# Optimization experiments

Hardware: AMD Instinct MI355X
Metric: run time of the kernel (lower is better)

The kernel has to match this reference:

```python
import jax, jax.numpy as jnp
import numpy as np

V = 8001
H = 512
B = 64
T = 129  # seq len; model unrolls T-1 steps
EPS = 1e-5
P_DROP = 0.3


def setup_inputs() -> dict:
    key = jax.random.key(0)
    ks = jax.random.split(key, 16)
    s = 1.0 / np.sqrt(H)
    inp = {
        "x": jax.random.randint(ks[0], (B, T), 0, V),
        "emb": jax.random.normal(ks[1], (V, H), jnp.float32) * 0.1,
        "W_ih1": jax.random.normal(ks[2], (4 * H, H), jnp.float32) * s,
        "W_hh1": jax.random.normal(ks[3], (4 * H, H), jnp.float32) * s,
        "b_ih1": jax.random.normal(ks[4], (4 * H,), jnp.float32) * s,
        "b_hh1": jax.random.normal(ks[5], (4 * H,), jnp.float32) * s,
        "gamma1": jnp.ones((H,), jnp.float32),
        "beta1": jnp.zeros((H,), jnp.float32),
        "mask1": (jax.random.bernoulli(ks[6], 1 - P_DROP, (B, H)).astype(jnp.float32) / (1 - P_DROP)),
        "W_ih2": jax.random.normal(ks[7], (4 * H, H), jnp.float32) * s,
        "W_hh2": jax.random.normal(ks[8], (4 * H, H), jnp.float32) * s,
        "b_ih2": jax.random.normal(ks[9], (4 * H,), jnp.float32) * s,
        "b_hh2": jax.random.normal(ks[10], (4 * H,), jnp.float32) * s,
        "gamma2": jnp.ones((H,), jnp.float32),
        "beta2": jnp.zeros((H,), jnp.float32),
        "mask2": (jax.random.bernoulli(ks[11], 1 - P_DROP, (B, H)).astype(jnp.float32) / (1 - P_DROP)),
        "W_dec": jax.random.normal(ks[12], (V, H), jnp.float32) * s,
        "b_dec": jax.random.normal(ks[13], (V,), jnp.float32) * s,
    }
    return inp


def _lstm_cell(xt, h, c, W_ih, W_hh, b_ih, b_hh):
    # PyTorch LSTMCell gate packing: i, f, g, o
    gates = xt @ W_ih.T + b_ih + h @ W_hh.T + b_hh  # [B, 4H]
    i, f, g, o = jnp.split(gates, 4, axis=-1)
    c_new = jax.nn.sigmoid(f) * c + jax.nn.sigmoid(i) * jnp.tanh(g)
    h_new = jax.nn.sigmoid(o) * jnp.tanh(c_new)
    return h_new, c_new


def _batchnorm(h, gamma, beta):
    # training-mode BatchNorm1d: biased batch stats over batch dim
    mu = h.mean(axis=0)
    var = h.var(axis=0)
    return gamma * (h - mu) * jax.lax.rsqrt(var + EPS) + beta


def reference(x, emb, W_ih1, W_hh1, b_ih1, b_hh1, gamma1, beta1, mask1,
              W_ih2, W_hh2, b_ih2, b_hh2, gamma2, beta2, mask2, W_dec, b_dec):
    embed = emb[x]                              # [B, T, H]
    xs = jnp.swapaxes(embed[:, :-1, :], 0, 1)   # [T-1, B, H]

    def step(carry, xt):
        h1, c1, h2, c2 = carry
        h1, c1 = _lstm_cell(xt, h1, c1, W_ih1, W_hh1, b_ih1, b_hh1)
        a = _batchnorm(h1, gamma1, beta1) * mask1
        h2, c2 = _lstm_cell(a, h2, c2, W_ih2, W_hh2, b_ih2, b_hh2)
        b = _batchnorm(h2, gamma2, beta2) * mask2
        out = b @ W_dec.T + b_dec               # [B, V]
        return (h1, c1, h2, c2), out

    z = jnp.zeros((B, H), embed.dtype)
    _, outs = jax.lax.scan(step, (z, z, z, z), xs)  # [T-1, B, V]
    return jnp.transpose(outs, (1, 2, 0))           # [B, V, T-1]
```

## Files before the change

kernel.cpp:

```cpp
#include <hip/hip_runtime.h>

typedef __attribute__((ext_vector_type(8))) short bf16x8;
typedef __attribute__((ext_vector_type(4))) float f32x4;

#define NBATCH 64
#define NH     512
#define NV     8001
#define NVP    8064
#define NSTEP  128
#define NG     2048
#define SLAB   32768

#define OFF_XS    ((size_t)0)
#define SZ_XS     ((size_t)NSTEP*SLAB*2)
#define OFF_WP    (OFF_XS + SZ_XS)
#define SZ_WP     ((size_t)2*2048*1024*2)
#define OFF_WDEC  (OFF_WP + SZ_WP)
#define SZ_WDEC   ((size_t)NVP*NH*2)
#define OFF_BIAS  (OFF_WDEC + SZ_WDEC)
#define SZ_BIAS   ((size_t)2*NG*4)
#define OFF_H1    (OFF_BIAS + SZ_BIAS)
#define SZ_H1     ((size_t)(NSTEP+1)*SLAB*2)
#define OFF_AB    (OFF_H1 + SZ_H1)
#define SZ_AB     ((size_t)NSTEP*SLAB*2)
#define OFF_H2    (OFF_AB + SZ_AB)
#define SZ_H2     ((size_t)(NSTEP+1)*SLAB*2)
#define OFF_BSEQ  (OFF_H2 + SZ_H2)
#define SZ_BSEQ   ((size_t)NSTEP*SLAB*2)
#define OFF_BAR   (OFF_BSEQ + SZ_BSEQ)
#define SZ_BAR    ((size_t)65536)

#define F_D1(t)   ((t) * 32)
#define F_D2(t)   (4096 + (t) * 32)
#define F_QCNT    8192
#define F_GBAR    8224
#define F_DRDY(c) (8320 + (c) * 32)

__device__ __forceinline__ unsigned short f2bf(float x) {
  union { float f; unsigned u; } v; v.f = x;
  unsigned r = v.u + 0x7FFFu + ((v.u >> 16) & 1u);
  return (unsigned short)(r >> 16);
}
__device__ __forceinline__ float sigm(float x) { return 1.f / (1.f + __expf(-x)); }

template <int SLP>
__device__ __forceinline__ void waitflag(unsigned* f) {
  while (__hip_atomic_load(f, __ATOMIC_RELAXED, __HIP_MEMORY_SCOPE_AGENT) < 32u)
    __builtin_amdgcn_s_sleep(SLP);
  asm volatile("" ::: "memory");
}

template <int SLP>
__device__ __forceinline__ void waitone(unsigned* f) {
  if (!__hip_atomic_load(f, __ATOMIC_RELAXED, __HIP_MEMORY_SCOPE_AGENT)) {
    do { __builtin_amdgcn_s_sleep(SLP); }
    while (!__hip_atomic_load(f, __ATOMIC_RELAXED, __HIP_MEMORY_SCOPE_AGENT));
  }
  asm volatile("" ::: "memory");
}

struct KArgs {
  const int* x; const float* emb;
  const float* Wih1; const float* Whh1; const float* bi1; const float* bh1;
  const float* g1; const float* be1; const float* m1;
  const float* Wih2; const float* Whh2; const float* bi2; const float* bh2;
  const float* g2; const float* be2; const float* m2;
  const float* Wdec; const float* bdec;
  unsigned short* xs; unsigned short* wp; unsigned short* wdec; float* bias;
  unsigned short* h1q; unsigned short* abq; unsigned short* h2q; unsigned short* bseq;
  unsigned* bar; float* out;
};

__global__ void __launch_bounds__(256, 1) k_main(KArgs a) {
  __shared__ unsigned short wlds[32 * 4 * 64 * 8];
  __shared__ float red[4][2][16];

  unsigned* bar = a.bar;
  const int bid = blockIdx.x;
  const int lane = threadIdx.x & 63, w = threadIdx.x >> 6;
  const int q = lane >> 4, n = lane & 15;

  {
    const int gtid = bid * 256 + threadIdx.x;
    if (gtid < 4096)
      a.bias[gtid] = (gtid < NG) ? (a.bi1[gtid] + a.bh1[gtid])
                                 : (a.bi2[gtid - NG] + a.bh2[gtid - NG]);
    if (gtid < 4096) {
      ((uint4*)a.h1q)[gtid] = (uint4){0, 0, 0, 0};
      ((uint4*)a.h2q)[gtid] = (uint4){0, 0, 0, 0};
    }
    for (int i = gtid; i < 524288; i += 65536) {
      int t = i >> 12, b = (i >> 6) & 63, h8 = i & 63;
      const float* src = a.emb + (size_t)a.x[b * 129 + t] * NH + h8 * 8;
      float4 u = *(const float4*)src, v = *(const float4*)(src + 4);
      unsigned short tmp[8] = {f2bf(u.x), f2bf(u.y), f2bf(u.z), f2bf(u.w),
                               f2bf(v.x), f2bf(v.y), f2bf(v.z), f2bf(v.w)};
      *(uint4*)(a.xs + (size_t)i * 8) = *(const uint4*)tmp;
    }
    for (int i = gtid; i < 516096; i += 65536) {
      int v = i >> 6, h8 = i & 63;
      unsigned short tmp[8] = {0, 0, 0, 0, 0, 0, 0, 0};
      if (v < NV) {
        const float* src = a.Wdec + (size_t)v * NH + h8 * 8;
        float4 u = *(const float4*)src, vv = *(const float4*)(src + 4);
        tmp[0] = f2bf(u.x); tmp[1] = f2bf(u.y); tmp[2] = f2bf(u.z); tmp[3] = f2bf(u.w);
        tmp[4] = f2bf(vv.x); tmp[5] = f2bf(vv.y); tmp[6] = f2bf(vv.z); tmp[7] = f2bf(vv.w);
      }
      *(uint4*)(a.wdec + (size_t)i * 8) = *(const uint4*)tmp;
    }
    for (int i = gtid; i < 524288; i += 65536) {
      int l = i & 63, g = (i >> 6) & 3, s = (i >> 8) & 31, lb = (i >> 13) & 31, layer = i >> 18;
      int nn = l & 15, qq = l >> 4;
      int r = g * NH + lb * 16 + nn;
      int k0 = s * 32 + qq * 8;
      const float* Wih = layer ? a.Wih2 : a.Wih1;
      const float* Whh = layer ? a.Whh2 : a.Whh1;
      const float* src = (k0 < NH) ? (Wih + (size_t)r * NH + k0) : (Whh + (size_t)r * NH + (k0 - NH));
      unsigned short tmp[8];
#pragma unroll
      for (int j = 0; j < 8; ++j) tmp[j] = f2bf(src[j]);
      *(uint4*)(a.wp + (size_t)i * 8) = *(const uint4*)tmp;
    }
  }
  __syncthreads();
  if (threadIdx.x == 0) {
    __builtin_amdgcn_fence(__ATOMIC_RELEASE, "agent");
    __hip_atomic_fetch_add(bar + F_GBAR, 1u, __ATOMIC_RELAXED, __HIP_MEMORY_SCOPE_AGENT);
    while (__hip_atomic_load(bar + F_GBAR, __ATOMIC_RELAXED, __HIP_MEMORY_SCOPE_AGENT) < 256u)
      __builtin_amdgcn_s_sleep(8);
  }
  __syncthreads();
  asm volatile("" ::: "memory");

  if (bid < 64) {
    const int layer = bid >> 5, lb = bid & 31, f0 = lb * 16;
    const float* gam = layer ? a.g2 : a.g1;
    const float* bet = layer ? a.be2 : a.be1;
    const float* msk = layer ? a.m2 : a.m1;
    const float* bias_l = a.bias + layer * NG;
    unsigned* myflag = bar + (layer ? F_D2(0) : F_D1(0));

    {
      const uint4* src = (const uint4*)(a.wp + (size_t)bid * (32 * 4 * 64 * 8));
      uint4* dst = (uint4*)wlds;
      for (int i = threadIdx.x; i < 32 * 4 * 64; i += 256) dst[i] = src[i];
    }
    __syncthreads();

    const int m0 = w * 16;
    const float gmv = gam[f0 + n], btv = bet[f0 + n];
    float bias_g[4], mk[4];
#pragma unroll
    for (int g = 0; g < 4; ++g) bias_g[g] = bias_l[g * NH + f0 + n];
#pragma unroll
    for (int r = 0; r < 4; ++r) mk[r] = msk[(m0 + q * 4 + r) * NH + f0 + n];

    float cst[4] = {0.f, 0.f, 0.f, 0.f};

    for (int t = 0; t < NSTEP; ++t) {
      f32x4 acc[4];
#pragma unroll
      for (int g = 0; g < 4; ++g) acc[g] = (f32x4){bias_g[g], bias_g[g], bias_g[g], bias_g[g]};

      if (layer == 0) {
        const unsigned short* rowA0 = a.xs + (size_t)t * SLAB + (m0 + n) * NH;
#pragma unroll
        for (int s = 0; s < 16; ++s) {
          bf16x8 af = *(const bf16x8*)(rowA0 + s * 32 + q * 8);
#pragma unroll
          for (int g = 0; g < 4; ++g)
            acc[g] = __builtin_amdgcn_mfma_f32_16x16x32_bf16(
                af, *(const bf16x8*)&wlds[((s * 4 + g) * 64 + lane) * 8], acc[g], 0, 0, 0);
        }
        if (t > 0) waitflag<1>(bar + F_D1(t - 1));
        const unsigned short* rowA1 = a.h1q + (size_t)t * SLAB + (m0 + n) * NH;
#pragma unroll
        for (int s = 0; s < 16; ++s) {
          bf16x8 af = *(const bf16x8*)(rowA1 + s * 32 + q * 8);
#pragma unroll
          for (int g = 0; g < 4; ++g)
            acc[g] = __builtin_amdgcn_mfma_f32_16x16x32_bf16(
                af, *(const bf16x8*)&wlds[(((s + 16) * 4 + g) * 64 + lane) * 8], acc[g], 0, 0, 0);
        }
      } else {
        if (t > 0) waitflag<1>(bar + F_D2(t - 1));
        const unsigned short* rowA1 = a.h2q + (size_t)t * SLAB + (m0 + n) * NH;
#pragma unroll
        for (int s = 0; s < 16; ++s) {
          bf16x8 af = *(const bf16x8*)(rowA1 + s * 32 + q * 8);
#pragma unroll
          for (int g = 0; g < 4; ++g)
            acc[g] = __builtin_amdgcn_mfma_f32_16x16x32_bf16(
                af, *(const bf16x8*)&wlds[(((s + 16) * 4 + g) * 64 + lane) * 8], acc[g], 0, 0, 0);
        }
        waitflag<1>(bar + F_D1(t));
        const unsigned short* rowA0 = a.abq + (size_t)t * SLAB + (m0 + n) * NH;
#pragma unroll
        for (int s = 0; s < 16; ++s) {
          bf16x8 af = *(const bf16x8*)(rowA0 + s * 32 + q * 8);
#pragma unroll
          for (int g = 0; g < 4; ++g)
            acc[g] = __builtin_amdgcn_mfma_f32_16x16x32_bf16(
                af, *(const bf16x8*)&wlds[((s * 4 + g) * 64 + lane) * 8], acc[g], 0, 0, 0);
        }
      }

      float hv[4], sum = 0.f, ssq = 0.f;
#pragma unroll
      for (int r = 0; r < 4; ++r) {
        float ig = sigm(acc[0][r]), fg = sigm(acc[1][r]);
        float gg = tanhf(acc[2][r]), og = sigm(acc[3][r]);
        cst[r] = fg * cst[r] + ig * gg;
        hv[r] = og * tanhf(cst[r]);
        sum += hv[r]; ssq += hv[r] * hv[r];
      }
      sum += __shfl_xor(sum, 16); ssq += __shfl_xor(ssq, 16);
      sum += __shfl_xor(sum, 32); ssq += __shfl_xor(ssq, 32);
      if (q == 0) { red[w][0][n] = sum; red[w][1][n] = ssq; }
      __syncthreads();
      float s1 = red[0][0][n] + red[1][0][n] + red[2][0][n] + red[3][0][n];
      float s2 = red[0][1][n] + red[1][1][n] + red[2][1][n] + red[3][1][n];
      float mu = s1 * (1.f / 64.f);
      float var = s2 * (1.f / 64.f) - mu * mu;
      float rs = rsqrtf(var + 1e-5f);

      unsigned short* hout = ((layer == 0) ? a.h1q : a.h2q) + (size_t)(t + 1) * SLAB;
      unsigned short* aout = ((layer == 0) ? a.abq : a.bseq) + (size_t)t * SLAB;
#pragma unroll
      for (int r = 0; r < 4; ++r) {
        int row = m0 + q * 4 + r;
        float bn = (hv[r] - mu) * rs * gmv + btv;
        unsigned short hb = f2bf(hv[r]);
        unsigned short av = f2bf(bn * mk[r]);
        __hip_atomic_store(&hout[row * NH + f0 + n], hb, __ATOMIC_RELAXED, __HIP_MEMORY_SCOPE_AGENT);
        __hip_atomic_store(&aout[row * NH + f0 + n], av, __ATOMIC_RELAXED, __HIP_MEMORY_SCOPE_AGENT);
      }

      __syncthreads();
      if (threadIdx.x == 0) {
        unsigned old = __hip_atomic_fetch_add(myflag + t * 32, 1u,
                                              __ATOMIC_RELAXED, __HIP_MEMORY_SCOPE_AGENT);
        if (layer == 1 && old == 31u && (t & 31) == 31)
          __hip_atomic_store(bar + F_DRDY(t >> 5), 1u,
                             __ATOMIC_RELAXED, __HIP_MEMORY_SCOPE_AGENT);
      }
    }
  }

  while (true) {
    unsigned c = 0;
    if (lane == 0) c = atomicAdd(bar + F_QCNT, 1u);
    c = __shfl(c, 0);
    if (c >= 16384u) break;
    unsigned tc = c >> 12, r = c & 4095u;
    if (r >= 4032u) continue;
    int nb = (int)(r >> 6), b = (int)(r & 63u);
    waitone<127>(bar + F_DRDY(tc));

    const int n0 = nb * 128;
    f32x4 acc[2][8];
#pragma unroll
    for (int nt = 0; nt < 8; ++nt) {
      int v = n0 + nt * 16 + n;
      float bd = (v < NV) ? a.bdec[v] : 0.f;
      acc[0][nt] = (f32x4){bd, bd, bd, bd};
      acc[1][nt] = acc[0][nt];
    }
    const unsigned short* arow[2];
#pragma unroll
    for (int mt = 0; mt < 2; ++mt)
      arow[mt] = a.bseq + ((size_t)(tc * 32 + mt * 16 + n) * NBATCH + b) * NH;
    const unsigned short* brow[8];
#pragma unroll
    for (int nt = 0; nt < 8; ++nt) brow[nt] = a.wdec + (size_t)(n0 + nt * 16 + n) * NH;

#pragma unroll 4
    for (int s = 0; s < 16; ++s) {
      bf16x8 af[2];
#pragma unroll
      for (int mt = 0; mt < 2; ++mt) af[mt] = *(const bf16x8*)(arow[mt] + s * 32 + q * 8);
#pragma unroll
      for (int nt = 0; nt < 8; ++nt) {
        bf16x8 bf = *(const bf16x8*)(brow[nt] + s * 32 + q * 8);
#pragma unroll
        for (int mt = 0; mt < 2; ++mt)
          acc[mt][nt] = __builtin_amdgcn_mfma_f32_16x16x32_bf16(af[mt], bf, acc[mt][nt], 0, 0, 0);
      }
    }
#pragma unroll
    for (int mt = 0; mt < 2; ++mt)
#pragma unroll
      for (int nt = 0; nt < 8; ++nt) {
        int v = n0 + nt * 16 + n;
        if (v < NV) {
          int t0 = (int)tc * 32 + mt * 16 + q * 4;
          *(f32x4*)(a.out + ((size_t)b * NV + v) * NSTEP + t0) = acc[mt][nt];
        }
      }
  }
}

extern "C" void kernel_launch(void* const* d_in, const int* in_sizes, int n_in,
                              void* d_out, int out_size, void* d_ws, size_t ws_size,
                              hipStream_t stream) {
  char* ws = (char*)d_ws;

  KArgs a;
  a.x    = (const int*)d_in[0];
  a.emb  = (const float*)d_in[1];
  a.Wih1 = (const float*)d_in[2];
  a.Whh1 = (const float*)d_in[3];
  a.bi1  = (const float*)d_in[4];
  a.bh1  = (const float*)d_in[5];
  a.g1   = (const float*)d_in[6];
  a.be1  = (const float*)d_in[7];
  a.m1   = (const float*)d_in[8];
  a.Wih2 = (const float*)d_in[9];
  a.Whh2 = (const float*)d_in[10];
  a.bi2  = (const float*)d_in[11];
  a.bh2  = (const float*)d_in[12];
  a.g2   = (const float*)d_in[13];
  a.be2  = (const float*)d_in[14];
  a.m2   = (const float*)d_in[15];
  a.Wdec = (const float*)d_in[16];
  a.bdec = (const float*)d_in[17];
  a.xs   = (unsigned short*)(ws + OFF_XS);
  a.wp   = (unsigned short*)(ws + OFF_WP);
  a.wdec = (unsigned short*)(ws + OFF_WDEC);
  a.bias = (float*)(ws + OFF_BIAS);
  a.h1q  = (unsigned short*)(ws + OFF_H1);
  a.abq  = (unsigned short*)(ws + OFF_AB);
  a.h2q  = (unsigned short*)(ws + OFF_H2);
  a.bseq = (unsigned short*)(ws + OFF_BSEQ);
  a.bar  = (unsigned*)(ws + OFF_BAR);
  a.out  = (float*)d_out;

  (void)hipMemsetAsync(a.bar, 0, SZ_BAR, stream);

  void* kargs[] = {(void*)&a};
  (void)hipLaunchCooperativeKernel((void*)k_main, dim3(256), dim3(256), kargs, 0, stream);
}
```

Measured before the change: 1.641 ms.

## Place each LSTM layer's blocks on one XCD and sync through local L2 flags

Each block reads its XCC hardware ID and claims a slot, so all 32 layer-1 blocks land on XCC 0 and all 32 layer-2 blocks on XCC 1. The hidden-state handoff inside a layer can then poll flags in the shared per-XCD L2 instead of going through device-scope atomics, with the agent-scope flag kept as a fallback. The h store and its flag are also split from the batchnorm/dropout output and published before the BN reduction finishes, so the next step's recurrent wait can clear sooner. This relies on undocumented L2 coherence behaviour (sc0 loads, non-atomic stores) and on how blocks are placed across XCDs, so it carries correctness risk, with the old mapping kept for when placement fails.

```diff
diff --git a/kernel.cpp b/kernel.cpp
--- a/kernel.cpp
+++ b/kernel.cpp
@@ -28,13 +28,17 @@
 #define OFF_BSEQ  (OFF_H2 + SZ_H2)
 #define SZ_BSEQ   ((size_t)NSTEP*SLAB*2)
 #define OFF_BAR   (OFF_BSEQ + SZ_BSEQ)
-#define SZ_BAR    ((size_t)65536)
-
-#define F_D1(t)   ((t) * 32)
-#define F_D2(t)   (4096 + (t) * 32)
-#define F_QCNT    8192
-#define F_GBAR    8224
-#define F_DRDY(c) (8320 + (c) * 32)
+#define SZ_BAR    ((size_t)131072)
+
+#define F_H1L(t)  ((t) * 32)
+#define F_H2L(t)  (4096 + (t) * 32)
+#define F_H1M(t)  (8192 + (t) * 32)
+#define F_H2M(t)  (12288 + (t) * 32)
+#define F_AB(t)   (16384 + (t) * 32)
+#define F_DC(c)   (20480 + (c) * 32)
+#define F_QCNT    20608
+#define F_GBAR    20640
+#define F_XCNT(x) (20672 + (x) * 32)
 
 __device__ __forceinline__ unsigned short f2bf(float x) {
   union { float f; unsigned u; } v; v.f = x;
@@ -43,19 +47,46 @@
 }
 __device__ __forceinline__ float sigm(float x) { return 1.f / (1.f + __expf(-x)); }
 
+__device__ __forceinline__ void l2_add(unsigned* p) {
+  unsigned one = 1u;
+  asm volatile("global_atomic_add %0, %1, off" :: "v"(p), "v"(one) : "memory");
+}
+__device__ __forceinline__ unsigned l2_load(unsigned* p) {
+  unsigned r;
+  asm volatile("global_load_dword %0, %1, off sc0\n\ts_waitcnt vmcnt(0)"
+               : "=v"(r) : "v"(p) : "memory");
+  return r;
+}
+__device__ __forceinline__ unsigned mall_load(unsigned* p) {
+  return __hip_atomic_load(p, __ATOMIC_RELAXED, __HIP_MEMORY_SCOPE_AGENT);
+}
+__device__ __forceinline__ void mall_add(unsigned* p) {
+  (void)__hip_atomic_fetch_add(p, 1u, __ATOMIC_RELAXED, __HIP_MEMORY_SCOPE_AGENT);
+}
+__device__ __forceinline__ void vm_drain() {
+  asm volatile("s_waitcnt vmcnt(0)" ::: "memory");
+}
+
+__device__ __forceinline__ void wait_h(unsigned* fl, unsigned* fm, bool fast) {
+  if (fast) {
+    while (true) {
+      bool hit = false;
+#pragma unroll
+      for (int i = 0; i < 8; ++i) {
+        if (l2_load(fl) >= 32u) { hit = true; break; }
+        __builtin_amdgcn_s_sleep(1);
+      }
+      if (hit) break;
+      if (mall_load(fm) >= 32u) break;
+    }
+  } else {
+    while (mall_load(fm) < 32u) __builtin_amdgcn_s_sleep(2);
+  }
+  asm volatile("" ::: "memory");
+}
 template <int SLP>
 __device__ __forceinline__ void waitflag(unsigned* f) {
-  while (__hip_atomic_load(f, __ATOMIC_RELAXED, __HIP_MEMORY_SCOPE_AGENT) < 32u)
-    __builtin_amdgcn_s_sleep(SLP);
-  asm volatile("" ::: "memory");
-}
-
-template <int SLP>
-__device__ __forceinline__ void waitone(unsigned* f) {
-  if (!__hip_atomic_load(f, __ATOMIC_RELAXED, __HIP_MEMORY_SCOPE_AGENT)) {
-    do { __builtin_amdgcn_s_sleep(SLP); }
-    while (!__hip_atomic_load(f, __ATOMIC_RELAXED, __HIP_MEMORY_SCOPE_AGENT));
-  }
+  while (mall_load(f) < 32u) __builtin_amdgcn_s_sleep(SLP);
   asm volatile("" ::: "memory");
 }
 
@@ -74,11 +105,26 @@
 __global__ void __launch_bounds__(256, 1) k_main(KArgs a) {
   __shared__ unsigned short wlds[32 * 4 * 64 * 8];
   __shared__ float red[4][2][16];
+  __shared__ int role_s, lb_s;
 
   unsigned* bar = a.bar;
   const int bid = blockIdx.x;
   const int lane = threadIdx.x & 63, w = threadIdx.x >> 6;
   const int q = lane >> 4, n = lane & 15;
+
+  if (threadIdx.x == 0) {
+    unsigned xcc;
+    asm volatile("s_getreg_b32 %0, hwreg(HW_REG_XCC_ID)" : "=s"(xcc));
+    xcc &= 7u;
+    unsigned slot = __hip_atomic_fetch_add(bar + F_XCNT(xcc), 1u,
+                                           __ATOMIC_RELAXED, __HIP_MEMORY_SCOPE_AGENT);
+    int role = 2, lb = 0;
+    if (slot < 32u) {
+      if (xcc == 0u) { role = 0; lb = (int)slot; }
+      else if (xcc == 1u) { role = 1; lb = (int)slot; }
+    }
+    role_s = role; lb_s = lb;
+  }
 
   {
     const int gtid = bid * 256 + threadIdx.x;
@@ -125,23 +171,29 @@
   __syncthreads();
   if (threadIdx.x == 0) {
     __builtin_amdgcn_fence(__ATOMIC_RELEASE, "agent");
-    __hip_atomic_fetch_add(bar + F_GBAR, 1u, __ATOMIC_RELAXED, __HIP_MEMORY_SCOPE_AGENT);
-    while (__hip_atomic_load(bar + F_GBAR, __ATOMIC_RELAXED, __HIP_MEMORY_SCOPE_AGENT) < 256u)
-      __builtin_amdgcn_s_sleep(8);
+    mall_add(bar + F_GBAR);
+    while (mall_load(bar + F_GBAR) < 256u) __builtin_amdgcn_s_sleep(8);
   }
   __syncthreads();
   asm volatile("" ::: "memory");
 
-  if (bid < 64) {
-    const int layer = bid >> 5, lb = bid & 31, f0 = lb * 16;
+  const bool fastlocal = (mall_load(bar + F_XCNT(0)) >= 32u) &&
+                         (mall_load(bar + F_XCNT(1)) >= 32u);
+  int role, lb;
+  if (fastlocal) { role = role_s; lb = lb_s; }
+  else           { role = (bid < 64) ? (bid >> 5) : 2; lb = bid & 31; }
+
+  if (role < 2) {
+    const int layer = role, f0 = lb * 16;
     const float* gam = layer ? a.g2 : a.g1;
     const float* bet = layer ? a.be2 : a.be1;
     const float* msk = layer ? a.m2 : a.m1;
     const float* bias_l = a.bias + layer * NG;
-    unsigned* myflag = bar + (layer ? F_D2(0) : F_D1(0));
+    unsigned* fL = bar + (layer ? F_H2L(0) : F_H1L(0));
+    unsigned* fM = bar + (layer ? F_H2M(0) : F_H1M(0));
 
     {
-      const uint4* src = (const uint4*)(a.wp + (size_t)bid * (32 * 4 * 64 * 8));
+      const uint4* src = (const uint4*)(a.wp + (size_t)(layer * 32 + lb) * (32 * 4 * 64 * 8));
       uint4* dst = (uint4*)wlds;
       for (int i = threadIdx.x; i < 32 * 4 * 64; i += 256) dst[i] = src[i];
     }
@@ -172,7 +224,7 @@
             acc[g] = __builtin_amdgcn_mfma_f32_16x16x32_bf16(
                 af, *(const bf16x8*)&wlds[((s * 4 + g) * 64 + lane) * 8], acc[g], 0, 0, 0);
         }
-        if (t > 0) waitflag<1>(bar + F_D1(t - 1));
+        if (t > 0) wait_h(fL + (t - 1) * 32, fM + (t - 1) * 32, fastlocal);
         const unsigned short* rowA1 = a.h1q + (size_t)t * SLAB + (m0 + n) * NH;
 #pragma unroll
         for (int s = 0; s < 16; ++s) {
@@ -183,7 +235,7 @@
                 af, *(const bf16x8*)&wlds[(((s + 16) * 4 + g) * 64 + lane) * 8], acc[g], 0, 0, 0);
         }
       } else {
-        if (t > 0) waitflag<1>(bar + F_D2(t - 1));
+        if (t > 0) wait_h(fL + (t - 1) * 32, fM + (t - 1) * 32, fastlocal);
         const unsigned short* rowA1 = a.h2q + (size_t)t * SLAB + (m0 + n) * NH;
 #pragma unroll
         for (int s = 0; s < 16; ++s) {
@@ -193,7 +245,7 @@
             acc[g] = __builtin_amdgcn_mfma_f32_16x16x32_bf16(
                 af, *(const bf16x8*)&wlds[(((s + 16) * 4 + g) * 64 + lane) * 8], acc[g], 0, 0, 0);
         }
-        waitflag<1>(bar + F_D1(t));
+        waitflag<2>(bar + F_AB(t));
         const unsigned short* rowA0 = a.abq + (size_t)t * SLAB + (m0 + n) * NH;
 #pragma unroll
         for (int s = 0; s < 16; ++s) {
@@ -214,35 +266,44 @@
         hv[r] = og * tanhf(cst[r]);
         sum += hv[r]; ssq += hv[r] * hv[r];
       }
+      unsigned short* hout = ((layer == 0) ? a.h1q : a.h2q) + (size_t)(t + 1) * SLAB;
+#pragma unroll
+      for (int r = 0; r < 4; ++r) {
+        unsigned short hb = f2bf(hv[r]);
+        if (fastlocal) hout[(m0 + q * 4 + r) * NH + f0 + n] = hb;
+        else __hip_atomic_store(&hout[(m0 + q * 4 + r) * NH + f0 + n], hb,
+                                __ATOMIC_RELAXED, __HIP_MEMORY_SCOPE_AGENT);
+      }
+
       sum += __shfl_xor(sum, 16); ssq += __shfl_xor(ssq, 16);
       sum += __shfl_xor(sum, 32); ssq += __shfl_xor(ssq, 32);
       if (q == 0) { red[w][0][n] = sum; red[w][1][n] = ssq; }
+      vm_drain();
       __syncthreads();
+      if (threadIdx.x == 0) {
+        if (fastlocal) l2_add(fL + t * 32);
+        mall_add(fM + t * 32);
+      }
+
       float s1 = red[0][0][n] + red[1][0][n] + red[2][0][n] + red[3][0][n];
       float s2 = red[0][1][n] + red[1][1][n] + red[2][1][n] + red[3][1][n];
       float mu = s1 * (1.f / 64.f);
       float var = s2 * (1.f / 64.f) - mu * mu;
       float rs = rsqrtf(var + 1e-5f);
 
-      unsigned short* hout = ((layer == 0) ? a.h1q : a.h2q) + (size_t)(t + 1) * SLAB;
       unsigned short* aout = ((layer == 0) ? a.abq : a.bseq) + (size_t)t * SLAB;
 #pragma unroll
       for (int r = 0; r < 4; ++r) {
-        int row = m0 + q * 4 + r;
         float bn = (hv[r] - mu) * rs * gmv + btv;
-        unsigned short hb = f2bf(hv[r]);
-        unsigned short av = f2bf(bn * mk[r]);
-        __hip_atomic_store(&hout[row * NH + f0 + n], hb, __ATOMIC_RELAXED, __HIP_MEMORY_SCOPE_AGENT);
-        __hip_atomic_store(&aout[row * NH + f0 + n], av, __ATOMIC_RELAXED, __HIP_MEMORY_SCOPE_AGENT);
-      }
-
+        __hip_atomic_store(&aout[(m0 + q * 4 + r) * NH + f0 + n], f2bf(bn * mk[r]),
+                           __ATOMIC_RELAXED, __HIP_MEMORY_SCOPE_AGENT);
+      }
+
+      vm_drain();
       __syncthreads();
       if (threadIdx.x == 0) {
-        unsigned old = __hip_atomic_fetch_add(myflag + t * 32, 1u,
-                                              __ATOMIC_RELAXED, __HIP_MEMORY_SCOPE_AGENT);
-        if (layer == 1 && old == 31u && (t & 31) == 31)
-          __hip_atomic_store(bar + F_DRDY(t >> 5), 1u,
-                             __ATOMIC_RELAXED, __HIP_MEMORY_SCOPE_AGENT);
+        if (layer == 0) mall_add(bar + F_AB(t));
+        else if ((t & 31) == 31) mall_add(bar + F_DC(t >> 5));
       }
     }
   }
@@ -255,7 +316,7 @@
     unsigned tc = c >> 12, r = c & 4095u;
     if (r >= 4032u) continue;
     int nb = (int)(r >> 6), b = (int)(r & 63u);
-    waitone<127>(bar + F_DRDY(tc));
+    waitflag<127>(bar + F_DC(tc));
 
     const int n0 = nb * 128;
     f32x4 acc[2][8];
```

Result: slower. 1.772 ms (+8.0%).
